# Kernel optimization log

Hardware: AMD Instinct MI355X
Metric: run time of the kernel (lower is better)

Reference implementation:

```python
import jax, jax.numpy as jnp
import numpy as np

B, H, W, C = 8, 256, 256, 32
WIN = 8
HEADS = 2
DH = C // HEADS          # 16
HIDDEN = 128             # mlp_ratio * C
N = WIN * WIN            # 64 tokens per window


def _rel_index(win):
    # standard Swin relative position index, computed once (static int constant)
    coords = np.stack(np.meshgrid(np.arange(win), np.arange(win), indexing='ij'))  # [2,w,w]
    coords = coords.reshape(2, -1)                                                  # [2,N]
    rel = (coords[:, :, None] - coords[:, None, :]).transpose(1, 2, 0)              # [N,N,2]
    rel[:, :, 0] += win - 1
    rel[:, :, 1] += win - 1
    rel[:, :, 0] *= 2 * win - 1
    return jnp.asarray(rel.sum(-1))                                                 # [N,N]

REL_IDX = _rel_index(WIN)


def setup_inputs() -> dict:
    key = jax.random.key(0)
    ks = jax.random.split(key, 10)
    rn = lambda k, s: jax.random.normal(k, s, jnp.float32) * 0.02
    return {
        'x': jax.random.normal(ks[0], (B, H * W, C), jnp.float32),
        'norm1_g': jnp.ones((C,), jnp.float32), 'norm1_b': jnp.zeros((C,), jnp.float32),
        'wq': rn(ks[1], (C, C)), 'bq': jnp.zeros((C,), jnp.float32),
        'wkv': rn(ks[2], (C, 2 * C)), 'bkv': jnp.zeros((2 * C,), jnp.float32),
        'wo': rn(ks[3], (C, C)), 'bo': jnp.zeros((C,), jnp.float32),
        'rel_bias': rn(ks[4], ((2 * WIN - 1) ** 2, HEADS)),
        'norm2_g': jnp.ones((C,), jnp.float32), 'norm2_b': jnp.zeros((C,), jnp.float32),
        'w1': rn(ks[5], (C, HIDDEN)), 'b1': jnp.zeros((HIDDEN,), jnp.float32),
        'dw': rn(ks[6], (HIDDEN, 1, 3, 3)), 'dwb': jnp.zeros((HIDDEN,), jnp.float32),
        'w2': rn(ks[7], (HIDDEN, C)), 'b2': jnp.zeros((C,), jnp.float32),
    }


def _ln(x, g, b):
    mu = x.mean(-1, keepdims=True)
    var = x.var(-1, keepdims=True)
    return (x - mu) / jnp.sqrt(var + 1e-5) * g + b


def _gelu(x):
    return jax.nn.gelu(x, approximate=False)  # torch nn.GELU is exact erf


def reference(x, norm1_g, norm1_b, wq, bq, wkv, bkv, wo, bo, rel_bias,
              norm2_g, norm2_b, w1, b1, dw, dwb, w2, b2):
    shortcut = x                                              # [B, HW, C]
    xn = _ln(x, norm1_g, norm1_b).reshape(B, H, W, C)
    # window partition -> [B*nW, N, C]
    xw = (xn.reshape(B, H // WIN, WIN, W // WIN, WIN, C)
            .transpose(0, 1, 3, 2, 4, 5)
            .reshape(-1, N, C))
    # linear qkv projection
    q = (xw @ wq + bq).reshape(-1, N, HEADS, DH).transpose(0, 2, 1, 3)      # [B_,h,N,d]
    kv = (xw @ wkv + bkv).reshape(-1, N, 2, HEADS, DH).transpose(2, 0, 3, 1, 4)
    k, v = kv[0], kv[1]
    scale = DH ** -0.5
    attn = jnp.einsum('bhnd,bhmd->bhnm', q * scale, k)                      # [B_,h,N,N]
    bias = rel_bias[REL_IDX].transpose(2, 0, 1)                             # [h,N,N]
    attn = jax.nn.softmax(attn + bias[None], axis=-1)
    out = jnp.einsum('bhnm,bhmd->bhnd', attn, v).transpose(0, 2, 1, 3).reshape(-1, N, C)
    out = out @ wo + bo
    # window reverse -> [B, HW, C]
    out = (out.reshape(B, H // WIN, W // WIN, WIN, WIN, C)
              .transpose(0, 1, 3, 2, 4, 5)
              .reshape(B, H * W, C))
    x = shortcut + out
    # LeFF: linear -> dwconv3x3 over full HxW map -> linear
    y = _ln(x, norm2_g, norm2_b)
    y = _gelu(y @ w1 + b1)                                                  # [B,HW,HIDDEN]
    y = y.reshape(B, H, W, HIDDEN).transpose(0, 3, 1, 2)                    # NCHW
    y = jax.lax.conv_general_dilated(
        y, dw, window_strides=(1, 1), padding='SAME',
        dimension_numbers=('NCHW', 'OIHW', 'NCHW'), feature_group_count=HIDDEN)
    y = _gelu(y + dwb[None, :, None, None])
    y = y.transpose(0, 2, 3, 1).reshape(B, H * W, HIDDEN)
    y = y @ w2 + b2
    return x + y
```

## Files before the change

kernel.cpp:

```cpp
#include <hip/hip_runtime.h>
#include <hip/hip_bf16.h>
#include <math.h>

#define IMG   256
#define HWTOK 65536
#define CH    32

typedef __attribute__((ext_vector_type(8))) _Float16 half8v;
typedef __attribute__((ext_vector_type(2))) _Float16 half2v;
typedef __attribute__((ext_vector_type(4))) float floatx4;

__device__ __forceinline__ unsigned short f2h(float f) {
    _Float16 h = (_Float16)f;
    return __builtin_bit_cast(unsigned short, h);
}
__device__ __forceinline__ float h2f(unsigned short u) {
    return (float)__builtin_bit_cast(_Float16, u);
}
__device__ __forceinline__ unsigned packh2(float a, float b) {
    return (unsigned)f2h(a) | ((unsigned)f2h(b) << 16);
}

__device__ __forceinline__ half2v gelu2v(half2v v) {
    const half2v hi = (half2v)(_Float16)( 2.0f);
    const half2v lo = (half2v)(_Float16)(-2.0f);
    const half2v vc = __builtin_elementwise_min(__builtin_elementwise_max(v, lo), hi);
    const half2v s  = vc * vc;
    half2v p = s * (half2v)(_Float16)(-1.18726e-3f) + (half2v)(_Float16)(9.97356e-3f);
    p = s * p + (half2v)(_Float16)(-6.64904e-2f);
    p = s * p + (half2v)(_Float16)( 3.989423e-1f);
    return v * (vc * p + (half2v)(_Float16)(0.5f));
}

__global__ __launch_bounds__(256) void attn_kernel(
    const float* __restrict__ x,
    const float* __restrict__ n1g, const float* __restrict__ n1b,
    const float* __restrict__ wq,  const float* __restrict__ bq,
    const float* __restrict__ wkv, const float* __restrict__ bkv,
    const float* __restrict__ wo,  const float* __restrict__ bo,
    const float* __restrict__ relb,
    float* __restrict__ x1)
{
    struct Win {
        union {
            unsigned short xn[64][40];
            unsigned short P[2][64][72];
            unsigned short O[64][40];
        } u;
        unsigned short Q[64][40];
        unsigned short K[64][56];
        unsigned short VT[2][16][72];
    };
    __shared__ Win W[2];
    __shared__ unsigned short bias16[2][228];
    __shared__ float denom[2][2][64];

    const int tid = threadIdx.x;
    const int wv  = tid >> 6;
    const int w   = wv >> 1;
    const int h   = wv & 1;
    const int l   = tid & 63;
    const int lm  = l & 15, lq = l >> 4;
    Win& S = W[w];

    const int win = blockIdx.x * 2 + w;
    const int b   = win >> 10;
    const int wh  = (win >> 5) & 31, ww = win & 31;
    const size_t wbase = ((size_t)b * HWTOK + (wh * 8) * IMG + ww * 8) * CH;

    const float LOG2E = 1.4426950408889634f;
    const float QSC   = 0.25f * LOG2E;

    half8v bwq, bwk, bwv, bwo0, bwo1;
    {
        const int lq8 = lq * 8;
        #pragma unroll
        for (int i = 0; i < 8; ++i) {
            bwq[i]  = (_Float16)(wq[(lq8 + i) * 32 + h * 16 + lm] * QSC);
            bwk[i]  = (_Float16)wkv[(lq8 + i) * 64 + h * 16 + lm];
            bwv[i]  = (_Float16)wkv[(lq8 + i) * 64 + 32 + h * 16 + lm];
            bwo0[i] = (_Float16)wo [(lq8 + i) * 32 + lm];
            bwo1[i] = (_Float16)wo [(lq8 + i) * 32 + 16 + lm];
        }
    }

    if (tid < 128) {
        const int sw = tid >> 6, st = tid & 63;
        Win& SS = W[sw];
        const int swin = blockIdx.x * 2 + sw;
        const int sb = swin >> 10, swh = (swin >> 5) & 31, sww = swin & 31;
        const size_t sbase = ((size_t)sb * HWTOK
                            + (swh * 8 + (st >> 3)) * IMG + sww * 8 + (st & 7)) * CH;
        const float4* xp = (const float4*)(x + sbase);
        float xr[32];
        float mu = 0.f;
        #pragma unroll
        for (int i = 0; i < 8; ++i) {
            const float4 v = xp[i];
            xr[i*4+0]=v.x; xr[i*4+1]=v.y; xr[i*4+2]=v.z; xr[i*4+3]=v.w;
            mu += v.x + v.y + v.z + v.w;
        }
        mu *= (1.f / 32.f);
        float var = 0.f;
        #pragma unroll
        for (int c = 0; c < 32; ++c) { const float d = xr[c] - mu; var += d * d; }
        const float inv = rsqrtf(var * (1.f / 32.f) + 1e-5f);
        unsigned int pk[16];
        #pragma unroll
        for (int j = 0; j < 16; ++j)
            pk[j] = packh2((xr[2*j]   - mu) * inv * n1g[2*j]   + n1b[2*j],
                           (xr[2*j+1] - mu) * inv * n1g[2*j+1] + n1b[2*j+1]);
        uint4* dst = (uint4*)&SS.u.xn[st][0];
        #pragma unroll
        for (int j = 0; j < 4; ++j) dst[j] = *(uint4*)&pk[j * 4];
        const uint4 z = {0u, 0u, 0u, 0u};
        *(uint4*)&SS.K[st][16] = z;
        *(uint4*)&SS.K[st][24] = z;
    } else {
        const int t2 = tid - 128;
        for (int i = t2; i < 450; i += 128) {
            const int hh = (i >= 225), r = i - hh * 225;
            bias16[hh][r] = f2h(relb[r * 2 + hh] * LOG2E);
        }
    }
    __syncthreads();

    const float bqv = bq[h*16 + lm] * QSC;
    const float bkv_ = bkv[h*16 + lm];
    const float bvv = bkv[32 + h*16 + lm];
    const floatx4 cq = {bqv, bqv, bqv, bqv};
    const floatx4 ck = {bkv_, bkv_, bkv_, bkv_};
    const floatx4 cv = {bvv, bvv, bvv, bvv};
    const floatx4 zero = {0.f, 0.f, 0.f, 0.f};

    #pragma unroll
    for (int mt = 0; mt < 4; ++mt) {
        const half8v a = *(const half8v*)&S.u.xn[mt*16 + lm][lq*8];
        const floatx4 dq = __builtin_amdgcn_mfma_f32_16x16x32_f16(a, bwq, cq, 0,0,0);
        const floatx4 dk = __builtin_amdgcn_mfma_f32_16x16x32_f16(a, bwk, ck, 0,0,0);
        const floatx4 dv = __builtin_amdgcn_mfma_f32_16x16x32_f16(a, bwv, cv, 0,0,0);
        const int r0 = mt*16 + lq*4;
        #pragma unroll
        for (int r = 0; r < 4; ++r) {
            S.Q[r0 + r][h*16 + lm] = f2h(dq[r]);
            S.K[r0 + r][h*32 + lm] = f2h(dk[r]);
        }
        uint2 vv;
        vv.x = packh2(dv[0], dv[1]);
        vv.y = packh2(dv[2], dv[3]);
        *(uint2*)&S.VT[h][lm][r0] = vv;
    }
    __syncthreads();

    half8v ak[4], bqf[4];
    #pragma unroll
    for (int mt = 0; mt < 4; ++mt)
        ak[mt] = *(const half8v*)&S.K[mt*16 + lm][h*16 + lq*8];
    #pragma unroll
    for (int nt = 0; nt < 4; ++nt)
        bqf[nt] = *(const half8v*)&S.Q[nt*16 + lm][lq*8];

    const int cc0 = (lm >> 3) * 15 + (lm & 7);
    const int cml = 15 * (lq >> 1) + 4 * (lq & 1);

    #pragma unroll
    for (int nt = 0; nt < 4; ++nt) {
        float sum = 0.f;
        const int base_nt = 30*nt + cc0 + 112 - cml;
        #pragma unroll
        for (int mt = 0; mt < 4; ++mt) {
            const floatx4 d = __builtin_amdgcn_mfma_f32_16x16x32_f16(ak[mt], bqf[nt], zero, 0,0,0);
            const int ib = base_nt - 30*mt;
            const float e0 = exp2f(d[0] + h2f(bias16[h][ib]));
            const float e1 = exp2f(d[1] + h2f(bias16[h][ib - 1]));
            const float e2 = exp2f(d[2] + h2f(bias16[h][ib - 2]));
            const float e3 = exp2f(d[3] + h2f(bias16[h][ib - 3]));
            sum += (e0 + e1) + (e2 + e3);
            uint2 pw;
            pw.x = packh2(e0, e1);
            pw.y = packh2(e2, e3);
            *(uint2*)&S.u.P[h][nt*16 + lm][mt*16 + lq*4] = pw;
        }
        sum += __shfl_xor(sum, 16);
        sum += __shfl_xor(sum, 32);
        if (l < 16) denom[w][h][nt*16 + l] = __frcp_rn(sum);
    }

    const half8v bva = *(const half8v*)&S.VT[h][lm][lq*8];
    const half8v bvb = *(const half8v*)&S.VT[h][lm][32 + lq*8];
    float oreg[16];
    #pragma unroll
    for (int mt = 0; mt < 4; ++mt) {
        const half8v ap0 = *(const half8v*)&S.u.P[h][mt*16 + lm][lq*8];
        const half8v ap1 = *(const half8v*)&S.u.P[h][mt*16 + lm][32 + lq*8];
        floatx4 ov = __builtin_amdgcn_mfma_f32_16x16x32_f16(ap0, bva, zero, 0,0,0);
        ov         = __builtin_amdgcn_mfma_f32_16x16x32_f16(ap1, bvb, ov,   0,0,0);
        const float4 dn = *(const float4*)&denom[w][h][mt*16 + lq*4];
        oreg[mt*4+0] = ov[0] * dn.x;
        oreg[mt*4+1] = ov[1] * dn.y;
        oreg[mt*4+2] = ov[2] * dn.z;
        oreg[mt*4+3] = ov[3] * dn.w;
    }
    __syncthreads();

    #pragma unroll
    for (int mt = 0; mt < 4; ++mt)
        #pragma unroll
        for (int r = 0; r < 4; ++r)
            S.u.O[mt*16 + lq*4 + r][h*16 + lm] = f2h(oreg[mt*4 + r]);
    __syncthreads();

    const float bo0 = bo[lm], bo1 = bo[16 + lm];
    const floatx4 co0 = {bo0, bo0, bo0, bo0};
    const floatx4 co1 = {bo1, bo1, bo1, bo1};
    #pragma unroll
    for (int mi = 0; mi < 2; ++mi) {
        const int mt = 2*h + mi;
        const half8v aO = *(const half8v*)&S.u.O[mt*16 + lm][lq*8];
        const floatx4 d0 = __builtin_amdgcn_mfma_f32_16x16x32_f16(aO, bwo0, co0, 0,0,0);
        const floatx4 d1 = __builtin_amdgcn_mfma_f32_16x16x32_f16(aO, bwo1, co1, 0,0,0);
        #pragma unroll
        for (int r = 0; r < 4; ++r) {
            const int t = mt*16 + lq*4 + r;
            const size_t g = wbase + (size_t)((t >> 3) * IMG + (t & 7)) * CH;
            x1[g + lm]      = x[g + lm]      + d0[r];
            x1[g + 16 + lm] = x[g + 16 + lm] + d1[r];
        }
    }
}

__global__ __launch_bounds__(256) void leff_kernel(
    const float* __restrict__ x1,
    const float* __restrict__ n2g, const float* __restrict__ n2b,
    const float* __restrict__ w1,  const float* __restrict__ b1,
    const float* __restrict__ dw,  const float* __restrict__ dwb,
    const float* __restrict__ w2,  const float* __restrict__ b2,
    float* __restrict__ out)
{
    union SharedU {
        struct { unsigned short xnA[112][40]; unsigned short w1T[128][40]; } p1;
        struct { unsigned short glA[64][136]; unsigned short w2T[32][136]; } p3;
    };
    __shared__ __align__(16) SharedU u;
    __shared__ __align__(16) unsigned short hid[100][136];

    const int blk = blockIdx.x;
    const int b = blk >> 10, tyb = (blk >> 5) & 31, txb = blk & 31;
    const int y0 = tyb * 8, x0 = txb * 8;
    const int tid = threadIdx.x;
    const int wv = tid >> 6;
    const int l  = tid & 63;
    const int lm = l & 15;
    const int lq = l >> 4;
    const bool edge = (tyb == 0) | (tyb == 31) | (txb == 0) | (txb == 31);

    if (tid < 200) {
        const int px = tid >> 1, half = tid & 1;
        const int hy = px / 10, hx = px % 10;
        const int iy = y0 + hy - 1, ix = x0 + hx - 1;
        const bool inb = (iy >= 0 && iy < IMG && ix >= 0 && ix < IMG);
        unsigned int pk[8];
        if (inb) {
            const size_t base = ((size_t)b * HWTOK + iy * IMG + ix) * CH + half * 16;
            const float4* xp = (const float4*)(x1 + base);
            float v[16];
            float s = 0.f;
            #pragma unroll
            for (int i = 0; i < 4; ++i) {
                const float4 t = xp[i];
                v[i*4+0]=t.x; v[i*4+1]=t.y; v[i*4+2]=t.z; v[i*4+3]=t.w;
                s += t.x + t.y + t.z + t.w;
            }
            const float mu = (s + __shfl_xor(s, 1)) * (1.f / 32.f);
            float q = 0.f;
            #pragma unroll
            for (int c = 0; c < 16; ++c) { const float d = v[c]-mu; q += d*d; }
            const float var = q + __shfl_xor(q, 1);
            const float inv = rsqrtf(var * (1.f/32.f) + 1e-5f);
            #pragma unroll
            for (int j = 0; j < 8; ++j) {
                const int c = half*16 + 2*j;
                pk[j] = packh2((v[2*j]   - mu) * inv * n2g[c]   + n2b[c],
                               (v[2*j+1] - mu) * inv * n2g[c+1] + n2b[c+1]);
            }
        } else {
            (void)__shfl_xor(0.f, 1); (void)__shfl_xor(0.f, 1);
            #pragma unroll
            for (int j = 0; j < 8; ++j) pk[j] = 0u;
        }
        uint4* dst = (uint4*)&u.p1.xnA[px][half * 16];
        dst[0] = *(uint4*)&pk[0];
        dst[1] = *(uint4*)&pk[4];
    } else if (tid < 248) {
        const int t2 = tid - 200;
        const uint4 z = {0u,0u,0u,0u};
        *(uint4*)&u.p1.xnA[100 + (t2 >> 2)][(t2 & 3) * 8] = z;
    }
    #pragma unroll
    for (int i = 0; i < 2; ++i) {
        const int o = tid + i * 256;
        const int row = o & 127, cq = o >> 7;
        const int bl = row >> 5, wi = row & 31;
        const int j = bl * 32 + ((wi & 15) << 1) + (wi >> 4);
        const int k0 = cq * 8;
        unsigned int pk4[4];
        #pragma unroll
        for (int jj = 0; jj < 4; ++jj)
            pk4[jj] = packh2(w1[(k0 + 2*jj) * 128 + j], w1[(k0 + 2*jj + 1) * 128 + j]);
        *(uint4*)&u.p1.w1T[row][k0] = *(uint4*)&pk4[0];
    }
    __syncthreads();

    {
        const int c0 = wv * 32 + 2 * lm;
        const half8v bf0 = *(const half8v*)&u.p1.w1T[wv * 32 + lm][lq * 8];
        const half8v bf1 = *(const half8v*)&u.p1.w1T[wv * 32 + 16 + lm][lq * 8];
        const float bias0 = b1[c0], bias1 = b1[c0 + 1];
        const floatx4 cb0 = {bias0, bias0, bias0, bias0};
        const floatx4 cb1 = {bias1, bias1, bias1, bias1};
        for (int mt = 0; mt < 7; ++mt) {
            const half8v af = *(const half8v*)&u.p1.xnA[mt * 16 + lm][lq * 8];
            floatx4 a0 = __builtin_amdgcn_mfma_f32_16x16x32_f16(af, bf0, cb0, 0, 0, 0);
            floatx4 a1 = __builtin_amdgcn_mfma_f32_16x16x32_f16(af, bf1, cb1, 0, 0, 0);
            #pragma unroll
            for (int r = 0; r < 4; ++r) {
                const int p = mt * 16 + lq * 4 + r;
                if (mt < 6 || p < 100) {
                    half2v hv;
                    hv.x = (_Float16)a0[r];
                    hv.y = (_Float16)a1[r];
                    half2v g = gelu2v(hv);
                    unsigned int bits = __builtin_bit_cast(unsigned int, g);
                    if (edge) {
                        const int hy = (p * 205) >> 11;
                        const int hx = p - hy * 10;
                        const int iy = y0 + hy - 1, ix = x0 + hx - 1;
                        const bool inb = (iy >= 0) & (iy < IMG) & (ix >= 0) & (ix < IMG);
                        if (!inb) bits = 0u;
                    }
                    *(unsigned int*)&hid[p][c0] = bits;
                }
            }
        }
    }
    __syncthreads();

    {
        const int jq = tid & 31, pg = tid >> 5;
        const int j0 = 4 * jq;
        half2v dwa[9], dwc[9];
        #pragma unroll
        for (int t = 0; t < 9; ++t) {
            dwa[t].x = (_Float16)dw[(j0    ) * 9 + t];
            dwa[t].y = (_Float16)dw[(j0 + 1) * 9 + t];
            dwc[t].x = (_Float16)dw[(j0 + 2) * 9 + t];
            dwc[t].y = (_Float16)dw[(j0 + 3) * 9 + t];
        }
        half2v dba, dbc;
        dba.x = (_Float16)dwb[j0];     dba.y = (_Float16)dwb[j0 + 1];
        dbc.x = (_Float16)dwb[j0 + 2]; dbc.y = (_Float16)dwb[j0 + 3];
        #pragma unroll
        for (int i = 0; i < 8; ++i) {
            const int p = pg * 8 + i;
            const int py = p >> 3, px = p & 7;
            half2v acca = dba, accc = dbc;
            #pragma unroll
            for (int ky = 0; ky < 3; ++ky)
                #pragma unroll
                for (int kx = 0; kx < 3; ++kx) {
                    const uint2 wrd =
                        *(const uint2*)&hid[(py + ky) * 10 + (px + kx)][j0];
                    acca = __builtin_bit_cast(half2v, wrd.x) * dwa[ky*3+kx] + acca;
                    accc = __builtin_bit_cast(half2v, wrd.y) * dwc[ky*3+kx] + accc;
                }
            const half2v ga = gelu2v(acca);
            const half2v gc = gelu2v(accc);
            uint2 ow;
            ow.x = __builtin_bit_cast(unsigned int, ga);
            ow.y = __builtin_bit_cast(unsigned int, gc);
            *(uint2*)&u.p3.glA[p][j0] = ow;
        }
        #pragma unroll
        for (int i = 0; i < 2; ++i) {
            const int o = tid + i * 256;
            const int c = o & 31, kq = o >> 5;
            const int k0 = kq * 8;
            unsigned int pk4[4];
            #pragma unroll
            for (int jj = 0; jj < 4; ++jj)
                pk4[jj] = packh2(w2[(k0 + 2*jj) * 32 + c], w2[(k0 + 2*jj + 1) * 32 + c]);
            *(uint4*)&u.p3.w2T[c][k0] = *(uint4*)&pk4[0];
        }
    }
    __syncthreads();

    {
        #pragma unroll
        for (int t = 0; t < 2; ++t) {
            const int idx = 2 * wv + t;
            const int mt = idx >> 1, nt = idx & 1;
            const int c = nt * 16 + lm;
            const float bias = b2[c];
            floatx4 acc = {bias, bias, bias, bias};
            #pragma unroll
            for (int kc = 0; kc < 4; ++kc) {
                const half8v a  = *(const half8v*)&u.p3.glA[mt * 16 + lm][kc * 32 + lq * 8];
                const half8v bb = *(const half8v*)&u.p3.w2T[nt * 16 + lm][kc * 32 + lq * 8];
                acc = __builtin_amdgcn_mfma_f32_16x16x32_f16(a, bb, acc, 0, 0, 0);
            }
            #pragma unroll
            for (int r = 0; r < 4; ++r) {
                const int p = mt * 16 + lq * 4 + r;
                const int iy = y0 + (p >> 3), ix = x0 + (p & 7);
                const size_t g = ((size_t)b * HWTOK + iy * IMG + ix) * CH + c;
                out[g] = x1[g] + acc[r];
            }
        }
    }
}

extern "C" void kernel_launch(void* const* d_in, const int* in_sizes, int n_in,
                              void* d_out, int out_size, void* d_ws, size_t ws_size,
                              hipStream_t stream)
{
    const float* x    = (const float*)d_in[0];
    const float* n1g  = (const float*)d_in[1];
    const float* n1b  = (const float*)d_in[2];
    const float* wq   = (const float*)d_in[3];
    const float* bq   = (const float*)d_in[4];
    const float* wkv  = (const float*)d_in[5];
    const float* bkv  = (const float*)d_in[6];
    const float* wo   = (const float*)d_in[7];
    const float* bo   = (const float*)d_in[8];
    const float* relb = (const float*)d_in[9];
    const float* n2g  = (const float*)d_in[10];
    const float* n2b  = (const float*)d_in[11];
    const float* w1   = (const float*)d_in[12];
    const float* b1   = (const float*)d_in[13];
    const float* dw   = (const float*)d_in[14];
    const float* dwb  = (const float*)d_in[15];
    const float* w2   = (const float*)d_in[16];
    const float* b2   = (const float*)d_in[17];

    float* out = (float*)d_out;
    float* x1  = (float*)d_ws;

    attn_kernel<<<4096, 256, 0, stream>>>(x, n1g, n1b, wq, bq, wkv, bkv,
                                          wo, bo, relb, x1);
    leff_kernel<<<8192, 256, 0, stream>>>(x1, n2g, n2b, w1, b1, dw, dwb,
                                          w2, b2, out);
}
```

Measured before the change: 159.5 us.

## Reuse dwconv row reads across pixels and raise LeFF occupancy hint

The depthwise 3x3 conv now loads each of the 3 halo rows (10 pixels) once per thread into registers and slides the window across 8 output pixels. Before, it did 9 shared loads per pixel, so this cuts LDS reads roughly 72 to 30. The kernel also gets a min-blocks-per-CU launch bound of 3 and a slightly narrower hid row stride, and drops dummy shuffles in the out-of-bounds path. The extra accumulator and row registers may pressure the register budget under the tighter launch bound. The new hid stride changes bank mapping and could add LDS conflicts.

New measurement: 154.8 us. -3.0%, faster.

```diff
diff --git a/kernel.cpp b/kernel.cpp
--- a/kernel.cpp
+++ b/kernel.cpp
@@ -229,7 +229,7 @@
     }
 }
 
-__global__ __launch_bounds__(256) void leff_kernel(
+__global__ __launch_bounds__(256, 3) void leff_kernel(
     const float* __restrict__ x1,
     const float* __restrict__ n2g, const float* __restrict__ n2b,
     const float* __restrict__ w1,  const float* __restrict__ b1,
@@ -242,7 +242,7 @@
         struct { unsigned short glA[64][136]; unsigned short w2T[32][136]; } p3;
     };
     __shared__ __align__(16) SharedU u;
-    __shared__ __align__(16) unsigned short hid[100][136];
+    __shared__ __align__(16) unsigned short hid[100][132];
 
     const int blk = blockIdx.x;
     const int b = blk >> 10, tyb = (blk >> 5) & 31, txb = blk & 31;
@@ -284,7 +284,6 @@
                                (v[2*j+1] - mu) * inv * n2g[c+1] + n2b[c+1]);
             }
         } else {
-            (void)__shfl_xor(0.f, 1); (void)__shfl_xor(0.f, 1);
             #pragma unroll
             for (int j = 0; j < 8; ++j) pk[j] = 0u;
         }
@@ -356,29 +355,36 @@
             dwc[t].x = (_Float16)dw[(j0 + 2) * 9 + t];
             dwc[t].y = (_Float16)dw[(j0 + 3) * 9 + t];
         }
-        half2v dba, dbc;
-        dba.x = (_Float16)dwb[j0];     dba.y = (_Float16)dwb[j0 + 1];
-        dbc.x = (_Float16)dwb[j0 + 2]; dbc.y = (_Float16)dwb[j0 + 3];
-        #pragma unroll
-        for (int i = 0; i < 8; ++i) {
-            const int p = pg * 8 + i;
-            const int py = p >> 3, px = p & 7;
-            half2v acca = dba, accc = dbc;
-            #pragma unroll
-            for (int ky = 0; ky < 3; ++ky)
+        half2v acca[8], accc[8];
+        {
+            half2v dba, dbc;
+            dba.x = (_Float16)dwb[j0];     dba.y = (_Float16)dwb[j0 + 1];
+            dbc.x = (_Float16)dwb[j0 + 2]; dbc.y = (_Float16)dwb[j0 + 3];
+            #pragma unroll
+            for (int i = 0; i < 8; ++i) { acca[i] = dba; accc[i] = dbc; }
+        }
+        #pragma unroll
+        for (int ky = 0; ky < 3; ++ky) {
+            uint2 rr[10];
+            #pragma unroll
+            for (int cx = 0; cx < 10; ++cx)
+                rr[cx] = *(const uint2*)&hid[(pg + ky) * 10 + cx][j0];
+            #pragma unroll
+            for (int i = 0; i < 8; ++i)
                 #pragma unroll
                 for (int kx = 0; kx < 3; ++kx) {
-                    const uint2 wrd =
-                        *(const uint2*)&hid[(py + ky) * 10 + (px + kx)][j0];
-                    acca = __builtin_bit_cast(half2v, wrd.x) * dwa[ky*3+kx] + acca;
-                    accc = __builtin_bit_cast(half2v, wrd.y) * dwc[ky*3+kx] + accc;
+                    acca[i] = __builtin_bit_cast(half2v, rr[i + kx].x) * dwa[ky*3+kx] + acca[i];
+                    accc[i] = __builtin_bit_cast(half2v, rr[i + kx].y) * dwc[ky*3+kx] + accc[i];
                 }
-            const half2v ga = gelu2v(acca);
-            const half2v gc = gelu2v(accc);
+        }
+        #pragma unroll
+        for (int i = 0; i < 8; ++i) {
+            const half2v ga = gelu2v(acca[i]);
+            const half2v gc = gelu2v(accc[i]);
             uint2 ow;
             ow.x = __builtin_bit_cast(unsigned int, ga);
             ow.y = __builtin_bit_cast(unsigned int, gc);
-            *(uint2*)&u.p3.glA[p][j0] = ow;
+            *(uint2*)&u.p3.glA[pg * 8 + i][j0] = ow;
         }
         #pragma unroll
         for (int i = 0; i < 2; ++i) {
```
